# Kernel tuning notes

Hardware: AMD Instinct MI355X
Metric: run time of the kernel (lower is better)

The kernel has to match this reference:

```python
import jax, jax.numpy as jnp
import numpy as np

U, I, D, NNZ, L = 100000, 50000, 64, 6000000, 3
N = U + I


def setup_inputs() -> dict:
    key = jax.random.key(0)
    ks = jax.random.split(key, 20)
    lin = lambda k: jax.random.normal(k, (D, D), jnp.float32) * (1.0 / np.sqrt(D))
    return {
        'user_emb': jax.random.normal(ks[0], (U, D), jnp.float32) * 0.02,
        'item_emb': jax.random.normal(ks[1], (I, D), jnp.float32) * 0.02,
        'edge_row': jax.random.randint(ks[2], (NNZ,), 0, N, jnp.int32),
        'edge_col': jax.random.randint(ks[3], (NNZ,), 0, N, jnp.int32),
        'edge_val': jax.random.uniform(ks[4], (NNZ,), jnp.float32) * (1.0 / 40.0),
        'W_sg1': lin(ks[5]), 'b_sg1': jnp.zeros((D,), jnp.float32),
        'W_sg2': lin(ks[6]), 'b_sg2': jnp.zeros((D,), jnp.float32),
        'W_uf1': lin(ks[7]), 'b_uf1': jnp.zeros((D,), jnp.float32),
        'W_uf2': lin(ks[8]), 'b_uf2': jnp.zeros((D,), jnp.float32),
        'W_if1': lin(ks[9]), 'b_if1': jnp.zeros((D,), jnp.float32),
        'W_if2': lin(ks[10]), 'b_if2': jnp.zeros((D,), jnp.float32),
    }


def _spmm(row, col, val, x):
    # sparse [N,N] @ dense [N,D] via gather + segment_sum (COO SpMM)
    return jax.ops.segment_sum(val[:, None] * x[col], row, num_segments=N)


def _linear(x, W, b):
    # torch nn.Linear: y = x @ W.T + b, W is [out, in]
    return x @ W.T + b


def reference(user_emb, item_emb, edge_row, edge_col, edge_val,
              W_sg1, b_sg1, W_sg2, b_sg2,
              W_uf1, b_uf1, W_uf2, b_uf2,
              W_if1, b_if1, W_if2, b_if2):
    ego = jnp.concatenate([user_emb, item_emb], axis=0)  # [N, D]
    acc = jnp.zeros_like(ego)
    for _ in range(L):  # perturbed=False path
        ego = _spmm(edge_row, edge_col, edge_val, ego)
        acc = acc + ego
    all_emb = acc / L  # mean over layers
    user_all, item_all = all_emb[:U], all_emb[U:]

    h_shared = _linear(jax.nn.relu(_linear(all_emb, W_sg1, b_sg1)), W_sg2, b_sg2)
    h_user = _linear(jax.nn.relu(_linear(user_all, W_uf1, b_uf1)), W_uf2, b_uf2)
    h_item = _linear(jax.nn.relu(_linear(item_all, W_if1, b_if1)), W_if2, b_if2)
    return (h_shared[:U], h_shared[U:], h_user, h_item)
```

## Files before the change

kernel.cpp:

```cpp
#include <hip/hip_runtime.h>
#include <hip/hip_bf16.h>

#define U_CNT 100000
#define I_CNT 50000
#define N_CNT 150000
#define NNZ_CNT 6000000
#define NBKT 1172
#define OFFW (NBKT + 1)
#define CHUNK 8192
#define NBLK_BIN 733
#define NGRP 147
#define COL_MASK 0x3FFFF

typedef unsigned short ushort_t;

__device__ __forceinline__ ushort_t f2bf_rne(float f) {
    unsigned u = __float_as_uint(f);
    unsigned r = (u + 0x7FFFu + ((u >> 16) & 1u)) >> 16;
    return (ushort_t)r;
}
__device__ __forceinline__ float bf2f(ushort_t h) {
    return __uint_as_float((unsigned)h << 16);
}

__global__ __launch_bounds__(1024) void bin_sort_kernel(
    const int* __restrict__ erow, const int* __restrict__ ecol,
    const float* __restrict__ evalv,
    int2* __restrict__ recs_bm, int* __restrict__ offM, int* __restrict__ gcnt)
{
    __shared__ int2 stage[CHUNK];
    __shared__ int  hist[NBKT];
    __shared__ int  lbase[NBKT];

    int t = threadIdx.x;
    int g = blockIdx.x;
    int base = g * CHUNK;
    int n = NNZ_CNT - base; if (n > CHUNK) n = CHUNK;

    for (int i = t; i < NBKT; i += 1024) hist[i] = 0;
    __syncthreads();

#pragma unroll
    for (int k = 0; k < 8; ++k) {
        int e = base + k * 1024 + t;
        if (e < NNZ_CNT) atomicAdd(&hist[erow[e] >> 7], 1);
    }
    __syncthreads();

    for (int i = t; i < NGRP; i += 1024) {
        int s = 0;
#pragma unroll
        for (int j = 0; j < 8; ++j) {
            int b = i * 8 + j;
            if (b < NBKT) s += hist[b];
        }
        if (s) atomicAdd(&gcnt[i], s);
    }

    int* sc = (int*)stage;
    int v0 = (t < NBKT) ? hist[t] : 0;
    int v1 = (1024 + t < NBKT) ? hist[1024 + t] : 0;
    sc[t] = v0; sc[1024 + t] = v1;
    __syncthreads();
    for (int off = 1; off < 1024; off <<= 1) {
        int u0 = (t >= off) ? sc[t - off] : 0;
        int u1 = (t >= off) ? sc[1024 + t - off] : 0;
        __syncthreads();
        sc[t] += u0; sc[1024 + t] += u1;
        __syncthreads();
    }
    int tot0 = sc[1023];
    if (t < NBKT) lbase[t] = sc[t] - v0;
    if (1024 + t < NBKT) lbase[1024 + t] = tot0 + sc[1024 + t] - v1;
    __syncthreads();

    for (int i = t; i < NBKT; i += 1024) hist[i] = 0;
    __syncthreads();

#pragma unroll
    for (int k = 0; k < 8; ++k) {
        int e = base + k * 1024 + t;
        if (e < NNZ_CNT) {
            int r = erow[e];
            int c = ecol[e];
            float v = evalv[e];
            int b = r >> 7;
            int p = lbase[b] + atomicAdd(&hist[b], 1);
            stage[p] = make_int2(((r & 16383) << 18) | c, __float_as_int(v));
        }
    }
    __syncthreads();

    for (int i = t; i < n; i += 1024) recs_bm[base + i] = stage[i];

    for (int i = t; i < NBKT; i += 1024)
        offM[(size_t)g * OFFW + i] = base + lbase[i];
    if (t == 0) offM[(size_t)g * OFFW + NBKT] = base + n;
}

__global__ __launch_bounds__(256) void gscan_kernel(
    const int* __restrict__ gcnt, int* __restrict__ gbase, int* __restrict__ rp)
{
    __shared__ int sm[256];
    int t = threadIdx.x;
    int v = (t < NGRP) ? gcnt[t] : 0;
    sm[t] = v;
    __syncthreads();
    for (int off = 1; off < 256; off <<= 1) {
        int u = (t >= off) ? sm[t - off] : 0;
        __syncthreads();
        sm[t] += u;
        __syncthreads();
    }
    if (t < NGRP) gbase[t] = sm[t] - v;
    if (t == 0) rp[N_CNT] = NNZ_CNT;
}

__global__ __launch_bounds__(1024) void build_csr_kernel(
    const int2* __restrict__ recs_bm, const int* __restrict__ offM,
    const int* __restrict__ gbase, int* __restrict__ rp,
    unsigned* __restrict__ pairs4)
{
    __shared__ int lcnt[1024];
    __shared__ int cur[1024];
    int t = threadIdx.x;
    int blk = blockIdx.x;
    int b0 = blk * 8;
    int bend = b0 + 8; if (bend > NBKT) bend = NBKT;

    lcnt[t] = 0;
    __syncthreads();

    int wid = t >> 6, lane = t & 63;

    for (int g = wid; g < NBLK_BIN; g += 16) {
        size_t o = (size_t)g * OFFW;
        int s = offM[o + b0], e = offM[o + bend];
        for (int i = s + lane; i < e; i += 64) {
            unsigned px = (unsigned)recs_bm[i].x;
            atomicAdd(&lcnt[(px >> 18) & 1023], 1);
        }
    }
    __syncthreads();

    int v = lcnt[t];
    __syncthreads();
    for (int off = 1; off < 1024; off <<= 1) {
        int u = (t >= off) ? lcnt[t - off] : 0;
        __syncthreads();
        lcnt[t] += u;
        __syncthreads();
    }
    int abs0 = gbase[blk] + lcnt[t] - v;
    cur[t] = abs0;
    int row = blk * 1024 + t;
    if (row < N_CNT) rp[row] = abs0;
    __syncthreads();

    for (int g = wid; g < NBLK_BIN; g += 16) {
        size_t o = (size_t)g * OFFW;
        int s = offM[o + b0], e = offM[o + bend];
        for (int i = s + lane; i < e; i += 64) {
            int2 rec = recs_bm[i];
            unsigned px = (unsigned)rec.x;
            unsigned col = px & COL_MASK;
            float val = __int_as_float(rec.y);
            unsigned v14 = (unsigned)(val * 655360.0f + 0.5f);
            if (v14 > 16383u) v14 = 16383u;
            int p = atomicAdd(&cur[(px >> 18) & 1023], 1);
            pairs4[p] = (col << 14) | v14;
        }
    }
}

__global__ __launch_bounds__(256) void cvt_concat_kernel(
    const float* __restrict__ ue, const float* __restrict__ ie,
    ushort_t* __restrict__ x0)
{
    const size_t UE = (size_t)U_CNT * 64;
    size_t i = ((size_t)blockIdx.x * 256 + threadIdx.x) * 8;
    if (i >= (size_t)N_CNT * 64) return;
    const float* src = (i < UE) ? (ue + i) : (ie + (i - UE));
    float4 a = *(const float4*)src;
    float4 b = *(const float4*)(src + 4);
    ushort_t o[8];
    o[0] = f2bf_rne(a.x); o[1] = f2bf_rne(a.y); o[2] = f2bf_rne(a.z); o[3] = f2bf_rne(a.w);
    o[4] = f2bf_rne(b.x); o[5] = f2bf_rne(b.y); o[6] = f2bf_rne(b.z); o[7] = f2bf_rne(b.w);
    *(uint4*)(x0 + i) = *(uint4*)o;
}

__global__ __launch_bounds__(256) void spmm_kernel(
    const int* __restrict__ rp, const unsigned* __restrict__ pairs4,
    const ushort_t* __restrict__ x, ushort_t* __restrict__ y)
{
    int wave = threadIdx.x >> 6;
    int lane = threadIdx.x & 63;
    int row = blockIdx.x * 4 + wave;
    if (row >= N_CNT) return;
    int s = __builtin_amdgcn_readfirstlane(rp[row]);
    int e = __builtin_amdgcn_readfirstlane(rp[row + 1]);
    const char* xb = (const char*)x;
    unsigned lane2 = (unsigned)(lane << 1);
    const float VQ = 1.52587890625e-06f;
    float sum = 0.f;
    int i = s;
    for (; i + 7 < e; i += 8) {
        unsigned p[8];
#pragma unroll
        for (int k = 0; k < 8; ++k) p[k] = pairs4[i + k];
        ushort_t a[8];
#pragma unroll
        for (int k = 0; k < 8; ++k)
            a[k] = *(const ushort_t*)(xb + (((p[k] & 0xFFFFC000u) >> 7) | lane2));
#pragma unroll
        for (int k = 0; k < 8; ++k)
            sum = fmaf((float)(p[k] & 16383u) * VQ, bf2f(a[k]), sum);
    }
    for (; i < e; ++i) {
        unsigned p = pairs4[i];
        ushort_t av = *(const ushort_t*)(xb + (((p & 0xFFFFC000u) >> 7) | lane2));
        sum = fmaf((float)(p & 16383u) * VQ, bf2f(av), sum);
    }
    y[(size_t)row * 64 + lane] = f2bf_rne(sum);
}

#define WST 68
__global__ __launch_bounds__(256) void mlp_dual_kernel(
    const ushort_t* __restrict__ x1p, const ushort_t* __restrict__ x2p,
    const ushort_t* __restrict__ x3p, int row_s, int row_e, float scale,
    const float* __restrict__ Ws1, const float* __restrict__ bs1,
    const float* __restrict__ Ws2, const float* __restrict__ bs2,
    const float* __restrict__ Wx1, const float* __restrict__ bx1,
    const float* __restrict__ Wx2, const float* __restrict__ bx2,
    float* __restrict__ out_s, float* __restrict__ out_x)
{
    __shared__ float S1[64 * WST], S2[64 * WST], X1[64 * WST], X2[64 * WST];
    __shared__ float rbuf[4][64], h1buf[4][64], h2buf[4][64];

    int t = threadIdx.x;
    for (int idx = t; idx < 4096; idx += 256) {
        int d = idx >> 6, k = idx & 63;
        S1[d * WST + k] = Ws1[idx];
        S2[d * WST + k] = Ws2[idx];
        X1[d * WST + k] = Wx1[idx];
        X2[d * WST + k] = Wx2[idx];
    }
    __syncthreads();

    int wave = t >> 6, lane = t & 63;
    float vbs1 = bs1[lane], vbs2 = bs2[lane];
    float vbx1 = bx1[lane], vbx2 = bx2[lane];
    const float4* s1v = (const float4*)&S1[lane * WST];
    const float4* s2v = (const float4*)&S2[lane * WST];
    const float4* x1v = (const float4*)&X1[lane * WST];
    const float4* x2v = (const float4*)&X2[lane * WST];

    for (int r = row_s + blockIdx.x * 4 + wave; r < row_e; r += gridDim.x * 4) {
        size_t o = (size_t)r * 64 + lane;
        float xv = (bf2f(x1p[o]) + bf2f(x2p[o]) + bf2f(x3p[o])) * scale;
        rbuf[wave][lane] = xv;
        float h1 = vbs1, h2 = vbx1;
#pragma unroll
        for (int k4 = 0; k4 < 16; ++k4) {
            float4 rv = *(const float4*)&rbuf[wave][k4 * 4];
            float4 w1 = s1v[k4];
            float4 w2 = x1v[k4];
            h1 = fmaf(rv.x, w1.x, h1); h1 = fmaf(rv.y, w1.y, h1);
            h1 = fmaf(rv.z, w1.z, h1); h1 = fmaf(rv.w, w1.w, h1);
            h2 = fmaf(rv.x, w2.x, h2); h2 = fmaf(rv.y, w2.y, h2);
            h2 = fmaf(rv.z, w2.z, h2); h2 = fmaf(rv.w, w2.w, h2);
        }
        h1 = fmaxf(h1, 0.f);
        h2 = fmaxf(h2, 0.f);
        h1buf[wave][lane] = h1;
        h2buf[wave][lane] = h2;
        float y1 = vbs2, y2 = vbx2;
#pragma unroll
        for (int k4 = 0; k4 < 16; ++k4) {
            float4 a1 = *(const float4*)&h1buf[wave][k4 * 4];
            float4 a2 = *(const float4*)&h2buf[wave][k4 * 4];
            float4 w1 = s2v[k4];
            float4 w2 = x2v[k4];
            y1 = fmaf(a1.x, w1.x, y1); y1 = fmaf(a1.y, w1.y, y1);
            y1 = fmaf(a1.z, w1.z, y1); y1 = fmaf(a1.w, w1.w, y1);
            y2 = fmaf(a2.x, w2.x, y2); y2 = fmaf(a2.y, w2.y, y2);
            y2 = fmaf(a2.z, w2.z, y2); y2 = fmaf(a2.w, w2.w, y2);
        }
        out_s[(size_t)r * 64 + lane] = y1;
        out_x[(size_t)r * 64 + lane] = y2;
    }
}


extern "C" void kernel_launch(void* const* d_in, const int* in_sizes, int n_in,
                              void* d_out, int out_size, void* d_ws, size_t ws_size,
                              hipStream_t stream)
{
    (void)in_sizes; (void)n_in; (void)out_size; (void)ws_size;

    const float* user_emb = (const float*)d_in[0];
    const float* item_emb = (const float*)d_in[1];
    const int*   erow     = (const int*)d_in[2];
    const int*   ecol     = (const int*)d_in[3];
    const float* evalv    = (const float*)d_in[4];
    const float* Wsg1 = (const float*)d_in[5];
    const float* bsg1 = (const float*)d_in[6];
    const float* Wsg2 = (const float*)d_in[7];
    const float* bsg2 = (const float*)d_in[8];
    const float* Wuf1 = (const float*)d_in[9];
    const float* buf1 = (const float*)d_in[10];
    const float* Wuf2 = (const float*)d_in[11];
    const float* buf2 = (const float*)d_in[12];
    const float* Wif1 = (const float*)d_in[13];
    const float* bif1 = (const float*)d_in[14];
    const float* Wif2 = (const float*)d_in[15];
    const float* bif2 = (const float*)d_in[16];

    float* out = (float*)d_out;
    const size_t XB = (size_t)N_CNT * 64;

    int2*     recs_bm = (int2*)out;
    int*      offM    = (int*)(out + 12000000);
    ushort_t* x0      = (ushort_t*)out;

    char* ws = (char*)d_ws;
    ushort_t* x1     = (ushort_t*)ws;
    ushort_t* x2     = x1 + XB;
    ushort_t* x3     = x2 + XB;
    unsigned* pairs4 = (unsigned*)(ws + XB * 6);
    int*      rp     = (int*)(ws + XB * 6 + (size_t)NNZ_CNT * 4);
    int*      gcnt   = rp + N_CNT + 8;
    int*      gbase  = gcnt + 160;

    hipMemsetAsync(gcnt, 0, NGRP * sizeof(int), stream);
    bin_sort_kernel<<<NBLK_BIN, 1024, 0, stream>>>(erow, ecol, evalv, recs_bm, offM, gcnt);
    gscan_kernel<<<1, 256, 0, stream>>>(gcnt, gbase, rp);
    build_csr_kernel<<<NGRP, 1024, 0, stream>>>(recs_bm, offM, gbase, rp, pairs4);

    cvt_concat_kernel<<<(int)((XB / 8 + 255) / 256), 256, 0, stream>>>(user_emb, item_emb, x0);

    int sg = N_CNT / 4;
    spmm_kernel<<<sg, 256, 0, stream>>>(rp, pairs4, x0, x1);
    spmm_kernel<<<sg, 256, 0, stream>>>(rp, pairs4, x1, x2);
    spmm_kernel<<<sg, 256, 0, stream>>>(rp, pairs4, x2, x3);

    const float sc = 1.0f / 3.0f;
    mlp_dual_kernel<<<512, 256, 0, stream>>>(x1, x2, x3, 0, U_CNT, sc,
        Wsg1, bsg1, Wsg2, bsg2, Wuf1, buf1, Wuf2, buf2, out, out + XB);
    mlp_dual_kernel<<<512, 256, 0, stream>>>(x1, x2, x3, U_CNT, N_CNT, sc,
        Wsg1, bsg1, Wsg2, bsg2, Wif1, bif1, Wif2, bif2, out, out + XB);
}
```

Measured before the change: 602.1 us.

## Rebuild COO-to-CSR as two-pass counting sort with global scans

Replaces the local bucket sort plus per-group gather CSR builder with a two-level counting sort. A per-source-chunk histogram over 1024-row groups is scanned globally so edges scatter straight to their group. A second pass then splits each group into two halves, histograms rows, scans a doubled row-pointer array and places the packed col/value words into final CSR order. This removes the build_csr kernel's strided walk over all 733 source chunks per group, at the cost of more kernel launches, an extra rowarr array, and only 294 blocks in the final placement.

Measured after the change: 646.3 us. 1.07x slower.

```diff
diff --git a/kernel.cpp b/kernel.cpp
--- a/kernel.cpp
+++ b/kernel.cpp
@@ -5,11 +5,10 @@
 #define I_CNT 50000
 #define N_CNT 150000
 #define NNZ_CNT 6000000
-#define NBKT 1172
-#define OFFW (NBKT + 1)
 #define CHUNK 8192
-#define NBLK_BIN 733
+#define NSRC 733
 #define NGRP 147
+#define GMN (NGRP * NSRC)
 #define COL_MASK 0x3FFFF
 
 typedef unsigned short ushort_t;
@@ -23,153 +22,132 @@
     return __uint_as_float((unsigned)h << 16);
 }
 
-__global__ __launch_bounds__(1024) void bin_sort_kernel(
-    const int* __restrict__ erow, const int* __restrict__ ecol,
-    const float* __restrict__ evalv,
-    int2* __restrict__ recs_bm, int* __restrict__ offM, int* __restrict__ gcnt)
-{
-    __shared__ int2 stage[CHUNK];
-    __shared__ int  hist[NBKT];
-    __shared__ int  lbase[NBKT];
-
-    int t = threadIdx.x;
-    int g = blockIdx.x;
-    int base = g * CHUNK;
-    int n = NNZ_CNT - base; if (n > CHUNK) n = CHUNK;
-
-    for (int i = t; i < NBKT; i += 1024) hist[i] = 0;
-    __syncthreads();
-
+__global__ __launch_bounds__(1024) void ghist_kernel(
+    const int* __restrict__ erow, int* __restrict__ gmat)
+{
+    __shared__ int h[NGRP];
+    int t = threadIdx.x;
+    int b = blockIdx.x;
+    if (t < NGRP) h[t] = 0;
+    __syncthreads();
+    int base = b * CHUNK;
 #pragma unroll
     for (int k = 0; k < 8; ++k) {
         int e = base + k * 1024 + t;
-        if (e < NNZ_CNT) atomicAdd(&hist[erow[e] >> 7], 1);
-    }
-    __syncthreads();
-
-    for (int i = t; i < NGRP; i += 1024) {
-        int s = 0;
-#pragma unroll
-        for (int j = 0; j < 8; ++j) {
-            int b = i * 8 + j;
-            if (b < NBKT) s += hist[b];
-        }
-        if (s) atomicAdd(&gcnt[i], s);
-    }
-
-    int* sc = (int*)stage;
-    int v0 = (t < NBKT) ? hist[t] : 0;
-    int v1 = (1024 + t < NBKT) ? hist[1024 + t] : 0;
-    sc[t] = v0; sc[1024 + t] = v1;
+        if (e < NNZ_CNT) atomicAdd(&h[erow[e] >> 10], 1);
+    }
+    __syncthreads();
+    if (t < NGRP) gmat[t * NSRC + b] = h[t];
+}
+
+__global__ void scan_block_kernel(const int* __restrict__ in, int* __restrict__ out,
+                                  int* __restrict__ bsum, int n) {
+    __shared__ int sm[1024];
+    int t = threadIdx.x;
+    int i = blockIdx.x * 1024 + t;
+    int v = (i < n) ? in[i] : 0;
+    sm[t] = v;
     __syncthreads();
     for (int off = 1; off < 1024; off <<= 1) {
-        int u0 = (t >= off) ? sc[t - off] : 0;
-        int u1 = (t >= off) ? sc[1024 + t - off] : 0;
+        int u = (t >= off) ? sm[t - off] : 0;
         __syncthreads();
-        sc[t] += u0; sc[1024 + t] += u1;
+        sm[t] += u;
         __syncthreads();
     }
-    int tot0 = sc[1023];
-    if (t < NBKT) lbase[t] = sc[t] - v0;
-    if (1024 + t < NBKT) lbase[1024 + t] = tot0 + sc[1024 + t] - v1;
-    __syncthreads();
-
-    for (int i = t; i < NBKT; i += 1024) hist[i] = 0;
-    __syncthreads();
-
+    if (i < n) out[i] = sm[t] - v;
+    if (t == 1023) bsum[blockIdx.x] = sm[1023];
+}
+
+__global__ void scan_small_kernel(int* __restrict__ bsum, int nb) {
+    __shared__ int sm[1024];
+    int t = threadIdx.x;
+    int v = (t < nb) ? bsum[t] : 0;
+    sm[t] = v;
+    __syncthreads();
+    for (int off = 1; off < 1024; off <<= 1) {
+        int u = (t >= off) ? sm[t - off] : 0;
+        __syncthreads();
+        sm[t] += u;
+        __syncthreads();
+    }
+    if (t < nb) bsum[t] = sm[t] - v;
+}
+
+__global__ void scan_fix_kernel(int* __restrict__ out, const int* __restrict__ boff,
+                                int n, int sent_idx, int sent_val) {
+    int i = blockIdx.x * 1024 + threadIdx.x;
+    if (i < n) out[i] += boff[blockIdx.x];
+    if (i == 0 && sent_idx >= 0) out[sent_idx] = sent_val;
+}
+
+__global__ __launch_bounds__(1024) void gplace_kernel(
+    const int* __restrict__ erow, const int* __restrict__ ecol,
+    const float* __restrict__ evalv, const int* __restrict__ gstart,
+    unsigned* __restrict__ pairarr, ushort_t* __restrict__ rowarr)
+{
+    __shared__ int cur[NGRP];
+    int t = threadIdx.x;
+    int b = blockIdx.x;
+    if (t < NGRP) cur[t] = gstart[t * NSRC + b];
+    __syncthreads();
+    int base = b * CHUNK;
 #pragma unroll
     for (int k = 0; k < 8; ++k) {
         int e = base + k * 1024 + t;
         if (e < NNZ_CNT) {
             int r = erow[e];
-            int c = ecol[e];
+            unsigned c = (unsigned)ecol[e];
             float v = evalv[e];
-            int b = r >> 7;
-            int p = lbase[b] + atomicAdd(&hist[b], 1);
-            stage[p] = make_int2(((r & 16383) << 18) | c, __float_as_int(v));
+            unsigned v14 = (unsigned)(v * 655360.0f + 0.5f);
+            if (v14 > 16383u) v14 = 16383u;
+            int p = atomicAdd(&cur[r >> 10], 1);
+            pairarr[p] = (c << 14) | v14;
+            rowarr[p]  = (ushort_t)(r & 1023);
         }
     }
-    __syncthreads();
-
-    for (int i = t; i < n; i += 1024) recs_bm[base + i] = stage[i];
-
-    for (int i = t; i < NBKT; i += 1024)
-        offM[(size_t)g * OFFW + i] = base + lbase[i];
-    if (t == 0) offM[(size_t)g * OFFW + NBKT] = base + n;
-}
-
-__global__ __launch_bounds__(256) void gscan_kernel(
-    const int* __restrict__ gcnt, int* __restrict__ gbase, int* __restrict__ rp)
-{
-    __shared__ int sm[256];
-    int t = threadIdx.x;
-    int v = (t < NGRP) ? gcnt[t] : 0;
-    sm[t] = v;
-    __syncthreads();
-    for (int off = 1; off < 256; off <<= 1) {
-        int u = (t >= off) ? sm[t - off] : 0;
-        __syncthreads();
-        sm[t] += u;
-        __syncthreads();
-    }
-    if (t < NGRP) gbase[t] = sm[t] - v;
-    if (t == 0) rp[N_CNT] = NNZ_CNT;
-}
-
-__global__ __launch_bounds__(1024) void build_csr_kernel(
-    const int2* __restrict__ recs_bm, const int* __restrict__ offM,
-    const int* __restrict__ gbase, int* __restrict__ rp,
+}
+
+__global__ __launch_bounds__(1024) void rhist2_kernel(
+    const ushort_t* __restrict__ rowarr, const int* __restrict__ gstart,
+    int* __restrict__ cnt2)
+{
+    __shared__ int cnt[1024];
+    int t = threadIdx.x;
+    int g = blockIdx.x >> 1;
+    int h = blockIdx.x & 1;
+    int s0 = gstart[g * NSRC];
+    int e0 = (g == NGRP - 1) ? NNZ_CNT : gstart[(g + 1) * NSRC];
+    int mid = (s0 + e0) >> 1;
+    int s = h ? mid : s0;
+    int e = h ? e0 : mid;
+    cnt[t] = 0;
+    __syncthreads();
+    for (int i = s + t; i < e; i += 1024) atomicAdd(&cnt[rowarr[i]], 1);
+    __syncthreads();
+    int row = g * 1024 + t;
+    if (row < N_CNT) cnt2[row * 2 + h] = cnt[t];
+}
+
+__global__ __launch_bounds__(1024) void place2_kernel(
+    const unsigned* __restrict__ pairarr, const ushort_t* __restrict__ rowarr,
+    const int* __restrict__ gstart, const int* __restrict__ rp2,
     unsigned* __restrict__ pairs4)
 {
-    __shared__ int lcnt[1024];
     __shared__ int cur[1024];
     int t = threadIdx.x;
-    int blk = blockIdx.x;
-    int b0 = blk * 8;
-    int bend = b0 + 8; if (bend > NBKT) bend = NBKT;
-
-    lcnt[t] = 0;
-    __syncthreads();
-
-    int wid = t >> 6, lane = t & 63;
-
-    for (int g = wid; g < NBLK_BIN; g += 16) {
-        size_t o = (size_t)g * OFFW;
-        int s = offM[o + b0], e = offM[o + bend];
-        for (int i = s + lane; i < e; i += 64) {
-            unsigned px = (unsigned)recs_bm[i].x;
-            atomicAdd(&lcnt[(px >> 18) & 1023], 1);
-        }
-    }
-    __syncthreads();
-
-    int v = lcnt[t];
-    __syncthreads();
-    for (int off = 1; off < 1024; off <<= 1) {
-        int u = (t >= off) ? lcnt[t - off] : 0;
-        __syncthreads();
-        lcnt[t] += u;
-        __syncthreads();
-    }
-    int abs0 = gbase[blk] + lcnt[t] - v;
-    cur[t] = abs0;
-    int row = blk * 1024 + t;
-    if (row < N_CNT) rp[row] = abs0;
-    __syncthreads();
-
-    for (int g = wid; g < NBLK_BIN; g += 16) {
-        size_t o = (size_t)g * OFFW;
-        int s = offM[o + b0], e = offM[o + bend];
-        for (int i = s + lane; i < e; i += 64) {
-            int2 rec = recs_bm[i];
-            unsigned px = (unsigned)rec.x;
-            unsigned col = px & COL_MASK;
-            float val = __int_as_float(rec.y);
-            unsigned v14 = (unsigned)(val * 655360.0f + 0.5f);
-            if (v14 > 16383u) v14 = 16383u;
-            int p = atomicAdd(&cur[(px >> 18) & 1023], 1);
-            pairs4[p] = (col << 14) | v14;
-        }
+    int g = blockIdx.x >> 1;
+    int h = blockIdx.x & 1;
+    int s0 = gstart[g * NSRC];
+    int e0 = (g == NGRP - 1) ? NNZ_CNT : gstart[(g + 1) * NSRC];
+    int mid = (s0 + e0) >> 1;
+    int s = h ? mid : s0;
+    int e = h ? e0 : mid;
+    int row = g * 1024 + t;
+    cur[t] = (row < N_CNT) ? rp2[row * 2 + h] : 0;
+    __syncthreads();
+    for (int i = s + t; i < e; i += 1024) {
+        int p = atomicAdd(&cur[rowarr[i]], 1);
+        pairs4[p] = pairarr[i];
     }
 }
 
@@ -190,15 +168,15 @@
 }
 
 __global__ __launch_bounds__(256) void spmm_kernel(
-    const int* __restrict__ rp, const unsigned* __restrict__ pairs4,
+    const int* __restrict__ rp2, const unsigned* __restrict__ pairs4,
     const ushort_t* __restrict__ x, ushort_t* __restrict__ y)
 {
     int wave = threadIdx.x >> 6;
     int lane = threadIdx.x & 63;
     int row = blockIdx.x * 4 + wave;
     if (row >= N_CNT) return;
-    int s = __builtin_amdgcn_readfirstlane(rp[row]);
-    int e = __builtin_amdgcn_readfirstlane(rp[row + 1]);
+    int s = __builtin_amdgcn_readfirstlane(rp2[2 * row]);
+    int e = __builtin_amdgcn_readfirstlane(rp2[2 * row + 2]);
     const char* xb = (const char*)x;
     unsigned lane2 = (unsigned)(lane << 1);
     const float VQ = 1.52587890625e-06f;
@@ -319,30 +297,43 @@
     float* out = (float*)d_out;
     const size_t XB = (size_t)N_CNT * 64;
 
-    int2*     recs_bm = (int2*)out;
-    int*      offM    = (int*)(out + 12000000);
-    ushort_t* x0      = (ushort_t*)out;
+    unsigned* pairarr = (unsigned*)out;
+    ushort_t* rowarr  = (ushort_t*)(out + 6000000);
+    ushort_t* x0      = (ushort_t*)(out + 9000000);
 
     char* ws = (char*)d_ws;
     ushort_t* x1     = (ushort_t*)ws;
     ushort_t* x2     = x1 + XB;
     ushort_t* x3     = x2 + XB;
     unsigned* pairs4 = (unsigned*)(ws + XB * 6);
-    int*      rp     = (int*)(ws + XB * 6 + (size_t)NNZ_CNT * 4);
-    int*      gcnt   = rp + N_CNT + 8;
-    int*      gbase  = gcnt + 160;
-
-    hipMemsetAsync(gcnt, 0, NGRP * sizeof(int), stream);
-    bin_sort_kernel<<<NBLK_BIN, 1024, 0, stream>>>(erow, ecol, evalv, recs_bm, offM, gcnt);
-    gscan_kernel<<<1, 256, 0, stream>>>(gcnt, gbase, rp);
-    build_csr_kernel<<<NGRP, 1024, 0, stream>>>(recs_bm, offM, gbase, rp, pairs4);
+    int*      rp2    = (int*)(ws + XB * 6 + (size_t)NNZ_CNT * 4);
+    int*      cnt2   = rp2 + 300008;
+    int*      gmat   = cnt2 + 300000;
+    int*      gstart = gmat + GMN + 8;
+    int*      bsumA  = gstart + GMN + 8;
+    int*      bsumD  = bsumA + 128;
+
+    const int NBA = (GMN + 1023) / 1024;
+    const int NBD = (300000 + 1023) / 1024;
+
+    ghist_kernel<<<NSRC, 1024, 0, stream>>>(erow, gmat);
+    scan_block_kernel<<<NBA, 1024, 0, stream>>>(gmat, gstart, bsumA, GMN);
+    scan_small_kernel<<<1, 1024, 0, stream>>>(bsumA, NBA);
+    scan_fix_kernel<<<NBA, 1024, 0, stream>>>(gstart, bsumA, GMN, GMN, NNZ_CNT);
+    gplace_kernel<<<NSRC, 1024, 0, stream>>>(erow, ecol, evalv, gstart, pairarr, rowarr);
+
+    rhist2_kernel<<<NGRP * 2, 1024, 0, stream>>>(rowarr, gstart, cnt2);
+    scan_block_kernel<<<NBD, 1024, 0, stream>>>(cnt2, rp2, bsumD, 300000);
+    scan_small_kernel<<<1, 1024, 0, stream>>>(bsumD, NBD);
+    scan_fix_kernel<<<NBD, 1024, 0, stream>>>(rp2, bsumD, 300000, 300000, NNZ_CNT);
+    place2_kernel<<<NGRP * 2, 1024, 0, stream>>>(pairarr, rowarr, gstart, rp2, pairs4);
 
     cvt_concat_kernel<<<(int)((XB / 8 + 255) / 256), 256, 0, stream>>>(user_emb, item_emb, x0);
 
     int sg = N_CNT / 4;
-    spmm_kernel<<<sg, 256, 0, stream>>>(rp, pairs4, x0, x1);
-    spmm_kernel<<<sg, 256, 0, stream>>>(rp, pairs4, x1, x2);
-    spmm_kernel<<<sg, 256, 0, stream>>>(rp, pairs4, x2, x3);
+    spmm_kernel<<<sg, 256, 0, stream>>>(rp2, pairs4, x0, x1);
+    spmm_kernel<<<sg, 256, 0, stream>>>(rp2, pairs4, x1, x2);
+    spmm_kernel<<<sg, 256, 0, stream>>>(rp2, pairs4, x2, x3);
 
     const float sc = 1.0f / 3.0f;
     mlp_dual_kernel<<<512, 256, 0, stream>>>(x1, x2, x3, 0, U_CNT, sc,
```
